# Kernel optimization log

Hardware: AMD Instinct MI355X
Metric: run time of the kernel (lower is better)

## Reference

```python
import jax, jax.numpy as jnp
import numpy as np

B, N, NODE_DIM, HID, HEAD = 32, 1024, 14, 64, 128
EDGE_PROB = 0.01


def setup_inputs() -> dict:
    key = jax.random.key(0)
    ks = jax.random.split(key, 12)
    x = jax.random.normal(ks[0], (B, N, NODE_DIM), dtype=jnp.float32)
    # sparse binary adjacency with self-loops (matches eye + edge scatter)
    adj = (jax.random.uniform(ks[1], (B, N, N)) < EDGE_PROB).astype(jnp.float32)
    adjacency = jnp.maximum(adj, jnp.eye(N, dtype=jnp.float32)[None])
    def lin(k, din, dout):
        kw, kb = jax.random.split(k)
        w = jax.random.normal(kw, (din, dout), dtype=jnp.float32) / np.sqrt(din)
        b = jnp.zeros((dout,), dtype=jnp.float32)
        return w, b
    W1, b1 = lin(ks[2], NODE_DIM, HID)
    W2, b2 = lin(ks[3], HID, HID)
    W3, b3 = lin(ks[4], HID, HID)
    Wf1, bf1 = lin(ks[5], HID, HEAD)
    Wf2, bf2 = lin(ks[6], HEAD, 1)
    return {"x": x, "adjacency": adjacency, "W1": W1, "b1": b1, "W2": W2,
            "b2": b2, "W3": W3, "b3": b3, "Wf1": Wf1, "bf1": bf1,
            "Wf2": Wf2, "bf2": bf2}


def _dense_graph_conv(x, norm_adj, W, b):
    # (D^-1/2 A D^-1/2) @ x, then linear
    return jnp.einsum('bnm,bmd->bnd', norm_adj, x) @ W + b


def reference(x, adjacency, W1, b1, W2, b2, W3, b3, Wf1, bf1, Wf2, bf2):
    degree = adjacency.sum(axis=-1)                      # [B,N]
    d_inv_sqrt = jnp.clip(degree, 1.0, None) ** -0.5
    norm_adj = d_inv_sqrt[..., :, None] * adjacency * d_inv_sqrt[..., None, :]
    h = jax.nn.relu(_dense_graph_conv(x, norm_adj, W1, b1))
    h = jax.nn.relu(_dense_graph_conv(h, norm_adj, W2, b2))
    h = jax.nn.relu(_dense_graph_conv(h, norm_adj, W3, b3))
    pooled = h.mean(axis=1)                              # [B,HID]
    return jax.nn.relu(pooled @ Wf1 + bf1) @ Wf2 + bf2   # [B,1]
```

## Files before the change

### kernel.cpp

```cpp
#include <hip/hip_runtime.h>
#include <math.h>

#define NN 1024
#define HID 64
#define HEADD 128
#define NODE_DIM 14
#define BATCH 32
#define CAP 64
#define ROWS (BATCH * NN)
#define RPW 8

__device__ __forceinline__ int swz4(int blk, int wv) {
    int x = blk & 7, q = blk >> 3;
    int batch = x + 8 * (q >> 8);
    return batch * NN + ((q & 255) << 2) + wv;
}
__device__ __forceinline__ int swz32(int blk, int wv) {
    int x = blk & 7, q = blk >> 3;
    int batch = x + 8 * (q >> 5);
    return batch * NN + ((q & 31) << 5) + wv * RPW;
}

__device__ __forceinline__ float rl_f(float v, int k) {
    return __int_as_float(__builtin_amdgcn_readlane(__float_as_int(v), k));
}

__global__ __launch_bounds__(256) void k_build(const float* __restrict__ adj,
                                               const float* __restrict__ x,
                                               const float* __restrict__ W1,
                                               unsigned short* __restrict__ csr,
                                               int* __restrict__ nnz_g,
                                               float* __restrict__ dinv,
                                               float* __restrict__ g1,
                                               float* __restrict__ pooled) {
    __shared__ float sW1[NODE_DIM * HID];
    for (int i = threadIdx.x; i < NODE_DIM * HID; i += 256) sW1[i] = W1[i];
    if (blockIdx.x < 8) pooled[blockIdx.x * 256 + threadIdx.x] = 0.f;
    int wv = threadIdx.x >> 6, lane = threadIdx.x & 63;
    int row = swz4(blockIdx.x, wv);
    const float4* rp = reinterpret_cast<const float4*>(adj + (size_t)row * NN);
    unsigned long long lt = ((unsigned long long)1 << lane) - 1;
    int base = 0;
#pragma unroll
    for (int j = 0; j < 4; ++j) {
        float4 v = rp[lane + 64 * j];
        float vv[4] = {v.x, v.y, v.z, v.w};
#pragma unroll
        for (int k = 0; k < 4; ++k) {
            unsigned long long mk = __ballot(vv[k] != 0.0f);
            if (mk) {
                if (vv[k] != 0.0f) {
                    int pos = base + __popcll(mk & lt);
                    if (pos < CAP)
                        csr[row * CAP + pos] = (unsigned short)((lane + 64 * j) * 4 + k);
                }
                base += __popcll(mk);
            }
        }
    }
    if (lane == 0) {
        nnz_g[row] = base < CAP ? base : CAP;
        dinv[row] = 1.0f / sqrtf((float)(base < 1 ? 1 : base));
    }
    __syncthreads();
    float acc = 0.f;
    const float* xr = x + (size_t)row * NODE_DIM;
#pragma unroll
    for (int d = 0; d < NODE_DIM; ++d) acc += xr[d] * sW1[d * HID + lane];
    g1[(size_t)row * HID + lane] = acc;
}

__device__ __forceinline__ void spmm8(const float* __restrict__ g_in,
                                      int bbase, const int n[RPW],
                                      const int idx[RPW], const float dv[RPW],
                                      int lane, float acc[RPW]) {
    int nmax = 0;
#pragma unroll
    for (int r = 0; r < RPW; ++r) { acc[r] = 0.f; nmax = n[r] > nmax ? n[r] : nmax; }
    for (int k = 0; k < nmax; ++k) {
        float w[RPW], v[RPW];
#pragma unroll
        for (int r = 0; r < RPW; ++r) {
            int j = __builtin_amdgcn_readlane(idx[r], k);
            w[r] = rl_f(dv[r], k);
            v[r] = g_in[(bbase + j) * HID + lane];
        }
#pragma unroll
        for (int r = 0; r < RPW; ++r) acc[r] += w[r] * v[r];
    }
}

__global__ __launch_bounds__(256, 4) void k_layer(const float* __restrict__ g_in,
                                                  const unsigned short* __restrict__ csr,
                                                  const int* __restrict__ nnz_g,
                                                  const float* __restrict__ dinv,
                                                  const float* __restrict__ bias,
                                                  const float* __restrict__ W,
                                                  float* __restrict__ g_out) {
    int wv = threadIdx.x >> 6, lane = threadIdx.x & 63;
    float wreg[HID];
#pragma unroll
    for (int d = 0; d < HID; ++d) wreg[d] = W[d * HID + lane];
    int row0 = swz32(blockIdx.x, wv);
    int bbase = row0 & ~(NN - 1);
    float bb = bias[lane];
    int n[RPW], idx[RPW];
    float dv[RPW];
#pragma unroll
    for (int r = 0; r < RPW; ++r) {
        int row = row0 + r;
        n[r] = __builtin_amdgcn_readfirstlane(nnz_g[row]);
        idx[r] = (lane < n[r]) ? (int)csr[row * CAP + lane] : 0;
        dv[r] = (lane < n[r]) ? dinv[bbase + idx[r]] : 0.f;
    }
    float acc[RPW];
    spmm8(g_in, bbase, n, idx, dv, lane, acc);
    float h[RPW];
#pragma unroll
    for (int r = 0; r < RPW; ++r)
        h[r] = fmaxf(dinv[row0 + r] * acc[r] + bb, 0.f);
    float o[RPW];
#pragma unroll
    for (int r = 0; r < RPW; ++r) o[r] = 0.f;
#pragma unroll
    for (int d = 0; d < HID; ++d) {
        float w = wreg[d];
#pragma unroll
        for (int r = 0; r < RPW; ++r) o[r] += rl_f(h[r], d) * w;
    }
#pragma unroll
    for (int r = 0; r < RPW; ++r)
        g_out[(size_t)(row0 + r) * HID + lane] = o[r];
}

__global__ __launch_bounds__(256, 4) void k_layer3(const float* __restrict__ g_in,
                                                   const unsigned short* __restrict__ csr,
                                                   const int* __restrict__ nnz_g,
                                                   const float* __restrict__ dinv,
                                                   const float* __restrict__ bias,
                                                   float* __restrict__ pooled) {
    __shared__ float sred[4][HID];
    int wv = threadIdx.x >> 6, lane = threadIdx.x & 63;
    int row0 = swz32(blockIdx.x, wv);
    int bbase = row0 & ~(NN - 1);
    float bb = bias[lane];
    int n[RPW], idx[RPW];
    float dv[RPW];
#pragma unroll
    for (int r = 0; r < RPW; ++r) {
        int row = row0 + r;
        n[r] = __builtin_amdgcn_readfirstlane(nnz_g[row]);
        idx[r] = (lane < n[r]) ? (int)csr[row * CAP + lane] : 0;
        dv[r] = (lane < n[r]) ? dinv[bbase + idx[r]] : 0.f;
    }
    float acc[RPW];
    spmm8(g_in, bbase, n, idx, dv, lane, acc);
    float s = 0.f;
#pragma unroll
    for (int r = 0; r < RPW; ++r)
        s += fmaxf(dinv[row0 + r] * acc[r] + bb, 0.f);
    sred[wv][lane] = s;
    __syncthreads();
    if (wv == 0) {
        float tot = sred[0][lane] + sred[1][lane] + sred[2][lane] + sred[3][lane];
        atomicAdd(&pooled[(bbase >> 10) * HID + lane], tot);
    }
}

__global__ __launch_bounds__(128) void k_head(const float* __restrict__ pooled_sum,
                                              const float* __restrict__ Wf1,
                                              const float* __restrict__ bf1,
                                              const float* __restrict__ Wf2,
                                              const float* __restrict__ bf2,
                                              float* __restrict__ out) {
    int b = blockIdx.x, t = threadIdx.x;
    __shared__ float p[HID];
    __shared__ float hid[HEADD];
    if (t < HID) p[t] = pooled_sum[b * HID + t] * (1.0f / NN);
    __syncthreads();
    float acc = bf1[t];
    for (int d = 0; d < HID; ++d) acc += p[d] * Wf1[d * HEADD + t];
    hid[t] = fmaxf(acc, 0.f);
    __syncthreads();
    if (t < 64) {
        float v = hid[t] * Wf2[t] + hid[t + 64] * Wf2[t + 64];
#pragma unroll
        for (int off = 32; off > 0; off >>= 1) v += __shfl_down(v, off, 64);
        if (t == 0) out[b] = v + bf2[0];
    }
}

extern "C" void kernel_launch(void* const* d_in, const int* in_sizes, int n_in,
                              void* d_out, int out_size, void* d_ws, size_t ws_size,
                              hipStream_t stream) {
    const float* x   = (const float*)d_in[0];
    const float* adj = (const float*)d_in[1];
    const float* W1  = (const float*)d_in[2];
    const float* b1  = (const float*)d_in[3];
    const float* W2  = (const float*)d_in[4];
    const float* b2  = (const float*)d_in[5];
    const float* W3  = (const float*)d_in[6];
    const float* b3  = (const float*)d_in[7];
    const float* Wf1 = (const float*)d_in[8];
    const float* bf1 = (const float*)d_in[9];
    const float* Wf2 = (const float*)d_in[10];
    const float* bf2 = (const float*)d_in[11];
    float* out = (float*)d_out;

    char* ws = (char*)d_ws;
    size_t off = 0;
    unsigned short* csr = (unsigned short*)(ws + off); off += (size_t)ROWS * CAP * 2;
    int*   nnz_g  = (int*)(ws + off);   off += (size_t)ROWS * 4;
    float* dinv   = (float*)(ws + off); off += (size_t)ROWS * 4;
    float* pooled = (float*)(ws + off); off += 4096 * 4;
    float* g1     = (float*)(ws + off); off += (size_t)ROWS * HID * 4;
    float* g2     = (float*)(ws + off); off += (size_t)ROWS * HID * 4;
    float* g3     = (float*)(ws + off);

    k_build <<<ROWS / 4, 256, 0, stream>>>(adj, x, W1, csr, nnz_g, dinv, g1, pooled);
    k_layer <<<ROWS / 32, 256, 0, stream>>>(g1, csr, nnz_g, dinv, b1, W2, g2);
    k_layer <<<ROWS / 32, 256, 0, stream>>>(g2, csr, nnz_g, dinv, b2, W3, g3);
    k_layer3<<<ROWS / 32, 256, 0, stream>>>(g3, csr, nnz_g, dinv, b3, pooled);
    k_head  <<<BATCH, 128, 0, stream>>>(pooled, Wf1, bf1, Wf2, bf2, out);
}
```

Measured before the change: 293.6 us.

## Split fused gather+GEMM layer kernels into separate gather and GEMM kernels

Each hidden layer kernel is split in two. One kernel does the sparse neighbor gather, normalization, bias and ReLU and writes h. The other does the 64x64 dense transform, reading h rows as uniform loads instead of cross-lane readlane broadcasts. The CSR indices widen from ushort to int and are read straight from global memory (uniform per row) rather than preloaded into lanes and fetched via readlane. This removes readlane-heavy inner loops and register pressure, but adds two extra kernel launches and an extra round trip of the full 8 MB activation buffer through memory per layer.

Measured after the change: 340.4 us. +15.9%, slower.

```diff
diff --git a/kernel.cpp b/kernel.cpp
--- a/kernel.cpp
+++ b/kernel.cpp
@@ -21,14 +21,10 @@
     return batch * NN + ((q & 31) << 5) + wv * RPW;
 }
 
-__device__ __forceinline__ float rl_f(float v, int k) {
-    return __int_as_float(__builtin_amdgcn_readlane(__float_as_int(v), k));
-}
-
 __global__ __launch_bounds__(256) void k_build(const float* __restrict__ adj,
                                                const float* __restrict__ x,
                                                const float* __restrict__ W1,
-                                               unsigned short* __restrict__ csr,
+                                               int* __restrict__ csr,
                                                int* __restrict__ nnz_g,
                                                float* __restrict__ dinv,
                                                float* __restrict__ g1,
@@ -51,8 +47,7 @@
             if (mk) {
                 if (vv[k] != 0.0f) {
                     int pos = base + __popcll(mk & lt);
-                    if (pos < CAP)
-                        csr[row * CAP + pos] = (unsigned short)((lane + 64 * j) * 4 + k);
+                    if (pos < CAP) csr[row * CAP + pos] = (lane + 64 * j) * 4 + k;
                 }
                 base += __popcll(mk);
             }
@@ -70,100 +65,124 @@
     g1[(size_t)row * HID + lane] = acc;
 }
 
-__device__ __forceinline__ void spmm8(const float* __restrict__ g_in,
-                                      int bbase, const int n[RPW],
-                                      const int idx[RPW], const float dv[RPW],
-                                      int lane, float acc[RPW]) {
-    int nmax = 0;
-#pragma unroll
-    for (int r = 0; r < RPW; ++r) { acc[r] = 0.f; nmax = n[r] > nmax ? n[r] : nmax; }
-    for (int k = 0; k < nmax; ++k) {
-        float w[RPW], v[RPW];
-#pragma unroll
-        for (int r = 0; r < RPW; ++r) {
-            int j = __builtin_amdgcn_readlane(idx[r], k);
-            w[r] = rl_f(dv[r], k);
-            v[r] = g_in[(bbase + j) * HID + lane];
-        }
-#pragma unroll
-        for (int r = 0; r < RPW; ++r) acc[r] += w[r] * v[r];
-    }
-}
-
-__global__ __launch_bounds__(256, 4) void k_layer(const float* __restrict__ g_in,
-                                                  const unsigned short* __restrict__ csr,
-                                                  const int* __restrict__ nnz_g,
-                                                  const float* __restrict__ dinv,
-                                                  const float* __restrict__ bias,
-                                                  const float* __restrict__ W,
-                                                  float* __restrict__ g_out) {
-    int wv = threadIdx.x >> 6, lane = threadIdx.x & 63;
-    float wreg[HID];
-#pragma unroll
-    for (int d = 0; d < HID; ++d) wreg[d] = W[d * HID + lane];
-    int row0 = swz32(blockIdx.x, wv);
-    int bbase = row0 & ~(NN - 1);
-    float bb = bias[lane];
-    int n[RPW], idx[RPW];
-    float dv[RPW];
-#pragma unroll
-    for (int r = 0; r < RPW; ++r) {
-        int row = row0 + r;
-        n[r] = __builtin_amdgcn_readfirstlane(nnz_g[row]);
-        idx[r] = (lane < n[r]) ? (int)csr[row * CAP + lane] : 0;
-        dv[r] = (lane < n[r]) ? dinv[bbase + idx[r]] : 0.f;
-    }
-    float acc[RPW];
-    spmm8(g_in, bbase, n, idx, dv, lane, acc);
-    float h[RPW];
-#pragma unroll
-    for (int r = 0; r < RPW; ++r)
-        h[r] = fmaxf(dinv[row0 + r] * acc[r] + bb, 0.f);
-    float o[RPW];
-#pragma unroll
-    for (int r = 0; r < RPW; ++r) o[r] = 0.f;
-#pragma unroll
-    for (int d = 0; d < HID; ++d) {
-        float w = wreg[d];
-#pragma unroll
-        for (int r = 0; r < RPW; ++r) o[r] += rl_f(h[r], d) * w;
-    }
-#pragma unroll
-    for (int r = 0; r < RPW; ++r)
-        g_out[(size_t)(row0 + r) * HID + lane] = o[r];
-}
-
-__global__ __launch_bounds__(256, 4) void k_layer3(const float* __restrict__ g_in,
-                                                   const unsigned short* __restrict__ csr,
+__global__ __launch_bounds__(256, 4) void k_gather(const float* __restrict__ g_in,
+                                                   const int* __restrict__ csr,
                                                    const int* __restrict__ nnz_g,
                                                    const float* __restrict__ dinv,
                                                    const float* __restrict__ bias,
-                                                   float* __restrict__ pooled) {
-    __shared__ float sred[4][HID];
-    int wv = threadIdx.x >> 6, lane = threadIdx.x & 63;
-    int row0 = swz32(blockIdx.x, wv);
+                                                   float* __restrict__ h_out) {
+    int wv = threadIdx.x >> 6, lane = threadIdx.x & 63;
+    int row0 = __builtin_amdgcn_readfirstlane(swz32(blockIdx.x, wv));
     int bbase = row0 & ~(NN - 1);
     float bb = bias[lane];
-    int n[RPW], idx[RPW];
-    float dv[RPW];
-#pragma unroll
-    for (int r = 0; r < RPW; ++r) {
-        int row = row0 + r;
-        n[r] = __builtin_amdgcn_readfirstlane(nnz_g[row]);
-        idx[r] = (lane < n[r]) ? (int)csr[row * CAP + lane] : 0;
-        dv[r] = (lane < n[r]) ? dinv[bbase + idx[r]] : 0.f;
+    int n[RPW];
+    int nmax = 0;
+#pragma unroll
+    for (int r = 0; r < RPW; ++r) {
+        n[r] = __builtin_amdgcn_readfirstlane(nnz_g[row0 + r]);
+        nmax = n[r] > nmax ? n[r] : nmax;
     }
     float acc[RPW];
-    spmm8(g_in, bbase, n, idx, dv, lane, acc);
+#pragma unroll
+    for (int r = 0; r < RPW; ++r) acc[r] = 0.f;
+    for (int k = 0; k < nmax; ++k) {
+        float w[RPW];
+        int jj[RPW];
+#pragma unroll
+        for (int r = 0; r < RPW; ++r) {
+            int jraw = csr[(row0 + r) * CAP + k];
+            int j = (k < n[r]) ? jraw : 0;
+            float dvj = dinv[bbase + j];
+            w[r] = (k < n[r]) ? dvj : 0.f;
+            jj[r] = j;
+        }
+        float v[RPW];
+#pragma unroll
+        for (int r = 0; r < RPW; ++r)
+            v[r] = g_in[(size_t)(bbase + jj[r]) * HID + lane];
+#pragma unroll
+        for (int r = 0; r < RPW; ++r) acc[r] += w[r] * v[r];
+    }
+#pragma unroll
+    for (int r = 0; r < RPW; ++r) {
+        float di = dinv[row0 + r];
+        h_out[(size_t)(row0 + r) * HID + lane] = fmaxf(di * acc[r] + bb, 0.f);
+    }
+}
+
+__global__ __launch_bounds__(256, 4) void k_gather3(const float* __restrict__ g_in,
+                                                    const int* __restrict__ csr,
+                                                    const int* __restrict__ nnz_g,
+                                                    const float* __restrict__ dinv,
+                                                    const float* __restrict__ bias,
+                                                    float* __restrict__ pooled) {
+    __shared__ float sred[4][HID];
+    int wv = threadIdx.x >> 6, lane = threadIdx.x & 63;
+    int row0 = __builtin_amdgcn_readfirstlane(swz32(blockIdx.x, wv));
+    int bbase = row0 & ~(NN - 1);
+    float bb = bias[lane];
+    int n[RPW];
+    int nmax = 0;
+#pragma unroll
+    for (int r = 0; r < RPW; ++r) {
+        n[r] = __builtin_amdgcn_readfirstlane(nnz_g[row0 + r]);
+        nmax = n[r] > nmax ? n[r] : nmax;
+    }
+    float acc[RPW];
+#pragma unroll
+    for (int r = 0; r < RPW; ++r) acc[r] = 0.f;
+    for (int k = 0; k < nmax; ++k) {
+        float w[RPW];
+        int jj[RPW];
+#pragma unroll
+        for (int r = 0; r < RPW; ++r) {
+            int jraw = csr[(row0 + r) * CAP + k];
+            int j = (k < n[r]) ? jraw : 0;
+            float dvj = dinv[bbase + j];
+            w[r] = (k < n[r]) ? dvj : 0.f;
+            jj[r] = j;
+        }
+        float v[RPW];
+#pragma unroll
+        for (int r = 0; r < RPW; ++r)
+            v[r] = g_in[(size_t)(bbase + jj[r]) * HID + lane];
+#pragma unroll
+        for (int r = 0; r < RPW; ++r) acc[r] += w[r] * v[r];
+    }
     float s = 0.f;
 #pragma unroll
-    for (int r = 0; r < RPW; ++r)
-        s += fmaxf(dinv[row0 + r] * acc[r] + bb, 0.f);
+    for (int r = 0; r < RPW; ++r) {
+        float di = dinv[row0 + r];
+        s += fmaxf(di * acc[r] + bb, 0.f);
+    }
     sred[wv][lane] = s;
     __syncthreads();
     if (wv == 0) {
         float tot = sred[0][lane] + sred[1][lane] + sred[2][lane] + sred[3][lane];
         atomicAdd(&pooled[(bbase >> 10) * HID + lane], tot);
+    }
+}
+
+__global__ __launch_bounds__(256, 4) void k_gemm(const float* __restrict__ h_in,
+                                                 const float* __restrict__ W,
+                                                 float* __restrict__ g_out) {
+    int wv = threadIdx.x >> 6, lane = threadIdx.x & 63;
+    float wreg[HID];
+#pragma unroll
+    for (int d = 0; d < HID; ++d) wreg[d] = W[d * HID + lane];
+    int row0 = __builtin_amdgcn_readfirstlane(swz32(blockIdx.x, wv));
+#pragma unroll
+    for (int r = 0; r < RPW; ++r) {
+        const float* hrow = h_in + (size_t)(row0 + r) * HID;
+        float o0 = 0.f, o1 = 0.f, o2 = 0.f, o3 = 0.f;
+#pragma unroll
+        for (int d = 0; d < HID; d += 4) {
+            o0 += hrow[d]     * wreg[d];
+            o1 += hrow[d + 1] * wreg[d + 1];
+            o2 += hrow[d + 2] * wreg[d + 2];
+            o3 += hrow[d + 3] * wreg[d + 3];
+        }
+        g_out[(size_t)(row0 + r) * HID + lane] = (o0 + o1) + (o2 + o3);
     }
 }
 
@@ -209,17 +228,18 @@
 
     char* ws = (char*)d_ws;
     size_t off = 0;
-    unsigned short* csr = (unsigned short*)(ws + off); off += (size_t)ROWS * CAP * 2;
+    int*   csr    = (int*)(ws + off);   off += (size_t)ROWS * CAP * 4;
     int*   nnz_g  = (int*)(ws + off);   off += (size_t)ROWS * 4;
     float* dinv   = (float*)(ws + off); off += (size_t)ROWS * 4;
     float* pooled = (float*)(ws + off); off += 4096 * 4;
-    float* g1     = (float*)(ws + off); off += (size_t)ROWS * HID * 4;
-    float* g2     = (float*)(ws + off); off += (size_t)ROWS * HID * 4;
-    float* g3     = (float*)(ws + off);
-
-    k_build <<<ROWS / 4, 256, 0, stream>>>(adj, x, W1, csr, nnz_g, dinv, g1, pooled);
-    k_layer <<<ROWS / 32, 256, 0, stream>>>(g1, csr, nnz_g, dinv, b1, W2, g2);
-    k_layer <<<ROWS / 32, 256, 0, stream>>>(g2, csr, nnz_g, dinv, b2, W3, g3);
-    k_layer3<<<ROWS / 32, 256, 0, stream>>>(g3, csr, nnz_g, dinv, b3, pooled);
-    k_head  <<<BATCH, 128, 0, stream>>>(pooled, Wf1, bf1, Wf2, bf2, out);
-}
+    float* gbuf   = (float*)(ws + off); off += (size_t)ROWS * HID * 4;
+    float* hbuf   = (float*)(ws + off);
+
+    k_build  <<<ROWS / 4, 256, 0, stream>>>(adj, x, W1, csr, nnz_g, dinv, gbuf, pooled);
+    k_gather <<<ROWS / 32, 256, 0, stream>>>(gbuf, csr, nnz_g, dinv, b1, hbuf);
+    k_gemm   <<<ROWS / 32, 256, 0, stream>>>(hbuf, W2, gbuf);
+    k_gather <<<ROWS / 32, 256, 0, stream>>>(gbuf, csr, nnz_g, dinv, b2, hbuf);
+    k_gemm   <<<ROWS / 32, 256, 0, stream>>>(hbuf, W3, gbuf);
+    k_gather3<<<ROWS / 32, 256, 0, stream>>>(gbuf, csr, nnz_g, dinv, b3, pooled);
+    k_head   <<<BATCH, 128, 0, stream>>>(pooled, Wf1, bf1, Wf2, bf2, out);
+}
```
